# Optimization experiments

Hardware: AMD Instinct MI355X
Metric: run time of the kernel (lower is better)

The kernel has to match this reference:

```python
import jax, jax.numpy as jnp
import numpy as np

T = 200000


def _sine_layer(tvec, A, w, phi, phic, wc):
    # tvec: (t,), A/w/phi: (n,1), phic/wc: (1,)
    phi_static = jax.nn.relu(phic)  # (1,)
    w_static = jax.nn.relu(wc)
    ph = jax.nn.relu(phi) + phi_static  # (n,1)
    ww = jax.nn.relu(w) + w_static
    sine = A * jnp.sin(ww * tvec[None, :] + ph)  # (n,t)
    return sine, phi_static, w_static


def _selector_layer(tvec, wave_input, w, phi, phic, wc, phi_prev, w_prev):
    # wave_input: (n,t), w/phi: (m,n), phic/wc/phi_prev/w_prev: (1,)
    # NOTE: phi_prev/w_prev passed but phi_prev flag is False in the network,
    # so they are NOT added (matches torch: `if self.phi_prev and ...`).
    phi_static = jax.nn.relu(phic)
    w_static = jax.nn.relu(wc)
    ph = (jax.nn.relu(phi) + phi_static)[:, :, None]  # (m,n,1)
    ww = (jax.nn.relu(w) + w_static)[:, :, None]
    sine = 0.5 * jnp.sin(ww * tvec[None, None, :] + ph) + 0.5  # (m,n,t)
    out = jnp.einsum('mnt,nt->mt', sine, wave_input)  # (m,t)
    return out, phi_static, w_static


def setup_inputs() -> dict:
    key = jax.random.key(0)
    ks = jax.random.split(key, 18)
    r = lambda k, s: jax.random.normal(k, s, dtype=jnp.float32)
    return {
        'initial_wave_input': r(ks[0], (20, T)),
        'A0': r(ks[1], (20, 1)), 'w0': r(ks[2], (20, 1)), 'phi0': r(ks[3], (20, 1)),
        'wc0': r(ks[4], (1,)), 'phic0': r(ks[5], (1,)),
        'w1': r(ks[6], (25, 20)), 'phi1': r(ks[7], (25, 20)),
        'wc1': r(ks[8], (1,)), 'phic1': r(ks[9], (1,)),
        'w2': r(ks[10], (30, 25)), 'phi2': r(ks[11], (30, 25)),
        'wc2': r(ks[12], (1,)), 'phic2': r(ks[13], (1,)),
        'w3': r(ks[14], (1, 30)), 'phi3': r(ks[15], (1, 30)),
        'wc3': r(ks[16], (1,)), 'phic3': r(ks[17], (1,)),
    }


def reference(initial_wave_input, A0, w0, phi0, wc0, phic0,
              w1, phi1, wc1, phic1, w2, phi2, wc2, phic2,
              w3, phi3, wc3, phic3):
    tvec = jnp.linspace(1.0, 1000.0, T, dtype=jnp.float32)
    # initial_wave_input is an argument of the torch module but is never used.
    s, phi, w = _sine_layer(tvec, A0, w0, phi0, phic0, wc0)
    s, phi, w = _selector_layer(tvec, s, w1, phi1, phic1, wc1, phi, w)
    s, phi, w = _selector_layer(tvec, s, w2, phi2, phic2, wc2, phi, w)
    s, phi, w = _selector_layer(tvec, s, w3, phi3, phic3, wc3, phi, w)
    return s  # (1, t)
```

## Files before the change

### kernel.cpp

```cpp
#include <hip/hip_runtime.h>
#include <hip/hip_bf16.h>

#define T_TOTAL 200000
#define T_PAD   200192
#define STEPF   (999.0f / 199999.0f)

typedef float v4f __attribute__((ext_vector_type(4)));

__device__ float g_P[5200];
__device__ float g_s1[25 * T_PAD];

__device__ __forceinline__ float sinp(float rev) {
    float g = __builtin_amdgcn_fractf(rev);
    float h = g - 0.5f;
    float u = h * h;
    float p = fmaf(45.621248f, u, -82.391040f);
    p = fmaf(p, u, 64.671616f);
    p = fmaf(p, u, -19.730960f);
    p = fmaf(p, u, 0.9999618f);
    return p;
}

__global__ void prep_kernel(
    const float* __restrict__ A0,
    const float* __restrict__ w0, const float* __restrict__ phi0,
    const float* __restrict__ wc0, const float* __restrict__ phic0,
    const float* __restrict__ w1, const float* __restrict__ phi1,
    const float* __restrict__ wc1, const float* __restrict__ phic1,
    const float* __restrict__ w2, const float* __restrict__ phi2,
    const float* __restrict__ wc2, const float* __restrict__ phic2,
    const float* __restrict__ w3, const float* __restrict__ phi3,
    const float* __restrict__ wc3, const float* __restrict__ phic3)
{
    const int tid = blockIdx.x * blockDim.x + threadIdx.x;
    const int stride = blockDim.x * gridDim.x;

    const double I2PI = 0.15915494309189535;
    const double D1   = 999.0 / 199999.0;

    const double ws0 = fmax((double)wc0[0], 0.0), ps0 = fmax((double)phic0[0], 0.0);
    const double ws1 = fmax((double)wc1[0], 0.0), ps1 = fmax((double)phic1[0], 0.0);
    const double ws2 = fmax((double)wc2[0], 0.0), ps2 = fmax((double)phic2[0], 0.0);
    const double ws3 = fmax((double)wc3[0], 0.0), ps3 = fmax((double)phic3[0], 0.0);

    for (int n = tid; n < 20; n += stride) {
        double wr = fmax((double)w0[n], 0.0) + ws0;
        g_P[4 * n]     = (float)(wr * I2PI);
        g_P[4 * n + 1] = (float)((fmax((double)phi0[n], 0.0) + ps0) * I2PI + 0.25);
        g_P[4 * n + 2] = (float)(2.0 * cos(wr * D1));
        g_P[4 * n + 3] = A0[n];
    }
    for (int k = tid; k < 25 * 20; k += stride) {
        double wr = fmax((double)w1[k], 0.0) + ws1;
        g_P[80 + 4 * k]     = (float)(wr * I2PI);
        g_P[80 + 4 * k + 1] = (float)((fmax((double)phi1[k], 0.0) + ps1) * I2PI + 0.25);
        g_P[80 + 4 * k + 2] = (float)(2.0 * cos(wr * D1));
        g_P[80 + 4 * k + 3] = 0.0f;
    }
    for (int k = tid; k < 30 * 25; k += stride) {
        double wr = fmax((double)w2[k], 0.0) + ws2;
        g_P[2080 + 4 * k]     = (float)(wr * I2PI);
        g_P[2080 + 4 * k + 1] = (float)((fmax((double)phi2[k], 0.0) + ps2) * I2PI + 0.25);
        g_P[2080 + 4 * k + 2] = (float)(2.0 * cos(wr * D1));
        g_P[2080 + 4 * k + 3] = 0.0f;
    }
    for (int m = tid; m < 30; m += stride) {
        double wr = fmax((double)w3[m], 0.0) + ws3;
        g_P[5080 + 4 * m]     = (float)(wr * I2PI);
        g_P[5080 + 4 * m + 1] = (float)((fmax((double)phi3[m], 0.0) + ps3) * I2PI + 0.25);
        g_P[5080 + 4 * m + 2] = (float)(2.0 * cos(wr * D1));
        g_P[5080 + 4 * m + 3] = 0.0f;
    }
}

__launch_bounds__(256)
__global__ void k_l01()
{
    __shared__ float pp[2000];
    __shared__ float s0s[20 * 256];

    const int tid = threadIdx.x;
    for (int i = tid; i < 2000; i += 256) pp[i] = g_P[80 + i];

    const int l = tid & 63;
    const int w = __builtin_amdgcn_readfirstlane(tid >> 6);
    const int tb = blockIdx.x * 256;
    const int tl = 4 * l;
    const float tv0 = fmaf((float)(tb + tl), STEPF, 1.0f);
    const float tv1 = tv0 + STEPF;

#pragma unroll
    for (int i = 0; i < 5; ++i) {
        const int n = 5 * w + i;
        const v4f q = *(const v4f*)&g_P[4 * n];
        float x0 = q[3] * sinp(fmaf(q[0], tv0, q[1]));
        float x1 = q[3] * sinp(fmaf(q[0], tv1, q[1]));
        float x2 = fmaf(q[2], x1, -x0);
        float x3 = fmaf(q[2], x2, -x1);
        *(v4f*)&s0s[n * 256 + tl] = (v4f){x0, x1, x2, x3};
    }
    __syncthreads();

    float sum0[4] = {0.f, 0.f, 0.f, 0.f};
#pragma unroll
    for (int n = 0; n < 20; ++n) {
        const v4f s = *(const v4f*)&s0s[n * 256 + tl];
        sum0[0] += s[0]; sum0[1] += s[1]; sum0[2] += s[2]; sum0[3] += s[3];
    }

    const int mS = w ? (1 + 6 * w) : 0;
    const int mC = w ? 6 : 7;
    for (int i = 0; i < mC; ++i) {
        const int m = mS + i;
        const float* __restrict__ pb = &pp[80 * m];
        float a0 = 0.f, a1 = 0.f, a2 = 0.f, a3 = 0.f;
#pragma unroll
        for (int n = 0; n < 20; ++n) {
            const v4f q = *(const v4f*)&pb[4 * n];
            const v4f s = *(const v4f*)&s0s[n * 256 + tl];
            float x0 = sinp(fmaf(q[0], tv0, q[1]));
            float x1 = sinp(fmaf(q[0], tv1, q[1]));
            float x2 = fmaf(q[2], x1, -x0);
            float x3 = fmaf(q[2], x2, -x1);
            a0 = fmaf(x0, s[0], a0);
            a1 = fmaf(x1, s[1], a1);
            a2 = fmaf(x2, s[2], a2);
            a3 = fmaf(x3, s[3], a3);
        }
        const v4f o = {fmaf(0.5f, a0, 0.5f * sum0[0]),
                       fmaf(0.5f, a1, 0.5f * sum0[1]),
                       fmaf(0.5f, a2, 0.5f * sum0[2]),
                       fmaf(0.5f, a3, 0.5f * sum0[3])};
        *(v4f*)&g_s1[m * T_PAD + tb + tl] = o;
    }
}

__launch_bounds__(256)
__global__ void k_l23(float* __restrict__ out)
{
    __shared__ float pp[3120];
    __shared__ float s1s[25 * 256];

    const int tid = threadIdx.x;
    const int tb = blockIdx.x * 256;
    for (int i = tid; i < 3120; i += 256) pp[i] = g_P[2080 + i];
    for (int i = tid; i < 25 * 256; i += 256)
        s1s[i] = g_s1[(i >> 8) * T_PAD + tb + (i & 255)];
    __syncthreads();

    const int l = tid & 63;
    const int w = __builtin_amdgcn_readfirstlane(tid >> 6);
    const int tl = 4 * l;
    const float tv0 = fmaf((float)(tb + tl), STEPF, 1.0f);
    const float tv1 = tv0 + STEPF;

    float sum1[4] = {0.f, 0.f, 0.f, 0.f};
#pragma unroll
    for (int n = 0; n < 25; ++n) {
        const v4f s = *(const v4f*)&s1s[n * 256 + tl];
        sum1[0] += s[0]; sum1[1] += s[1]; sum1[2] += s[2]; sum1[3] += s[3];
    }

    const int mS = (w < 2) ? 8 * w : (16 + 7 * (w - 2));
    const int mC = (w < 2) ? 8 : 7;
    float pw0 = 0.f, pw1 = 0.f, pw2 = 0.f, pw3 = 0.f;
    for (int i = 0; i < mC; ++i) {
        const int m = mS + i;
        const float* __restrict__ pb = &pp[100 * m];
        float a0 = 0.f, a1 = 0.f, a2 = 0.f, a3 = 0.f;
#pragma unroll
        for (int n = 0; n < 25; ++n) {
            const v4f q = *(const v4f*)&pb[4 * n];
            const v4f s = *(const v4f*)&s1s[n * 256 + tl];
            float x0 = sinp(fmaf(q[0], tv0, q[1]));
            float x1 = sinp(fmaf(q[0], tv1, q[1]));
            float x2 = fmaf(q[2], x1, -x0);
            float x3 = fmaf(q[2], x2, -x1);
            a0 = fmaf(x0, s[0], a0);
            a1 = fmaf(x1, s[1], a1);
            a2 = fmaf(x2, s[2], a2);
            a3 = fmaf(x3, s[3], a3);
        }
        const v4f q3 = *(const v4f*)&pp[3000 + 4 * m];
        float y0 = sinp(fmaf(q3[0], tv0, q3[1]));
        float y1 = sinp(fmaf(q3[0], tv1, q3[1]));
        float y2 = fmaf(q3[2], y1, -y0);
        float y3 = fmaf(q3[2], y2, -y1);
        pw0 = fmaf(fmaf(0.5f, y0, 0.5f), fmaf(0.5f, a0, 0.5f * sum1[0]), pw0);
        pw1 = fmaf(fmaf(0.5f, y1, 0.5f), fmaf(0.5f, a1, 0.5f * sum1[1]), pw1);
        pw2 = fmaf(fmaf(0.5f, y2, 0.5f), fmaf(0.5f, a2, 0.5f * sum1[2]), pw2);
        pw3 = fmaf(fmaf(0.5f, y3, 0.5f), fmaf(0.5f, a3, 0.5f * sum1[3]), pw3);
    }
    __syncthreads();
    float* const shp = pp;
    *(v4f*)&shp[w * 256 + tl] = (v4f){pw0, pw1, pw2, pw3};
    __syncthreads();

    const int tlr = 64 * w + l;
    const float r = (shp[0 * 256 + tlr] + shp[1 * 256 + tlr])
                  + (shp[2 * 256 + tlr] + shp[3 * 256 + tlr]);
    const int tt = tb + tlr;
    if (tt < T_TOTAL) out[tt] = r;
}

extern "C" void kernel_launch(void* const* d_in, const int* in_sizes, int n_in,
                              void* d_out, int out_size, void* d_ws, size_t ws_size,
                              hipStream_t stream) {
    (void)in_sizes; (void)n_in; (void)d_ws; (void)ws_size; (void)out_size;
    const float* A0    = (const float*)d_in[1];
    const float* w0    = (const float*)d_in[2];
    const float* phi0  = (const float*)d_in[3];
    const float* wc0   = (const float*)d_in[4];
    const float* phic0 = (const float*)d_in[5];
    const float* w1    = (const float*)d_in[6];
    const float* phi1  = (const float*)d_in[7];
    const float* wc1   = (const float*)d_in[8];
    const float* phic1 = (const float*)d_in[9];
    const float* w2    = (const float*)d_in[10];
    const float* phi2  = (const float*)d_in[11];
    const float* wc2   = (const float*)d_in[12];
    const float* phic2 = (const float*)d_in[13];
    const float* w3    = (const float*)d_in[14];
    const float* phi3  = (const float*)d_in[15];
    const float* wc3   = (const float*)d_in[16];
    const float* phic3 = (const float*)d_in[17];

    float* out = (float*)d_out;

    hipLaunchKernelGGL(prep_kernel, dim3(6), dim3(256), 0, stream,
                       A0, w0, phi0, wc0, phic0,
                       w1, phi1, wc1, phic1,
                       w2, phi2, wc2, phic2,
                       w3, phi3, wc3, phic3);

    const int grid = (T_TOTAL + 255) / 256;
    hipLaunchKernelGGL(k_l01, dim3(grid), dim3(256), 0, stream);
    hipLaunchKernelGGL(k_l23, dim3(grid), dim3(256), 0, stream, out);
}
```

Measured before the change: 64.68 us.

## Split layer-2/3 kernel across two blocks per tile and combine partials

Each 256-element time tile of the layer-2/3 kernel is now handled by two blocks, each covering 15 of the 30 layer-2 outputs, with per-half partial sums written to a global buffer and added by a new combine kernel. The s1 tile is read directly from global memory instead of being staged in LDS, which shrinks shared memory use and should allow more resident blocks. This doubles the grid to fill more CUs, at the cost of an extra kernel launch, an extra global round trip for the partial sums, and redundant global loads of s1.

```diff
diff --git a/kernel.cpp b/kernel.cpp
--- a/kernel.cpp
+++ b/kernel.cpp
@@ -9,6 +9,7 @@
 
 __device__ float g_P[5200];
 __device__ float g_s1[25 * T_PAD];
+__device__ float g_part[2 * T_PAD];
 
 __device__ __forceinline__ float sinp(float rev) {
     float g = __builtin_amdgcn_fractf(rev);
@@ -136,17 +137,18 @@
 }
 
 __launch_bounds__(256)
-__global__ void k_l23(float* __restrict__ out)
-{
-    __shared__ float pp[3120];
-    __shared__ float s1s[25 * 256];
+__global__ void k_l23()
+{
+    __shared__ float pp[1560];
+    __shared__ float shp[4 * 256];
 
     const int tid = threadIdx.x;
-    const int tb = blockIdx.x * 256;
-    for (int i = tid; i < 3120; i += 256) pp[i] = g_P[2080 + i];
-    for (int i = tid; i < 25 * 256; i += 256)
-        s1s[i] = g_s1[(i >> 8) * T_PAD + tb + (i & 255)];
-    __syncthreads();
+    const int half = blockIdx.x & 1;
+    const int tb = (blockIdx.x >> 1) * 256;
+
+    for (int i = tid; i < 1560; i += 256)
+        pp[i] = (i < 1500) ? g_P[2080 + 1500 * half + i]
+                           : g_P[5080 + 60 * half + (i - 1500)];
 
     const int l = tid & 63;
     const int w = __builtin_amdgcn_readfirstlane(tid >> 6);
@@ -157,21 +159,22 @@
     float sum1[4] = {0.f, 0.f, 0.f, 0.f};
 #pragma unroll
     for (int n = 0; n < 25; ++n) {
-        const v4f s = *(const v4f*)&s1s[n * 256 + tl];
+        const v4f s = *(const v4f*)&g_s1[n * T_PAD + tb + tl];
         sum1[0] += s[0]; sum1[1] += s[1]; sum1[2] += s[2]; sum1[3] += s[3];
     }
-
-    const int mS = (w < 2) ? 8 * w : (16 + 7 * (w - 2));
-    const int mC = (w < 2) ? 8 : 7;
+    __syncthreads();
+
+    const int mS = 4 * w;
+    const int mC = (w == 3) ? 3 : 4;
     float pw0 = 0.f, pw1 = 0.f, pw2 = 0.f, pw3 = 0.f;
     for (int i = 0; i < mC; ++i) {
-        const int m = mS + i;
-        const float* __restrict__ pb = &pp[100 * m];
+        const int lm = mS + i;
+        const float* __restrict__ pb = &pp[100 * lm];
         float a0 = 0.f, a1 = 0.f, a2 = 0.f, a3 = 0.f;
 #pragma unroll
         for (int n = 0; n < 25; ++n) {
             const v4f q = *(const v4f*)&pb[4 * n];
-            const v4f s = *(const v4f*)&s1s[n * 256 + tl];
+            const v4f s = *(const v4f*)&g_s1[n * T_PAD + tb + tl];
             float x0 = sinp(fmaf(q[0], tv0, q[1]));
             float x1 = sinp(fmaf(q[0], tv1, q[1]));
             float x2 = fmaf(q[2], x1, -x0);
@@ -181,7 +184,7 @@
             a2 = fmaf(x2, s[2], a2);
             a3 = fmaf(x3, s[3], a3);
         }
-        const v4f q3 = *(const v4f*)&pp[3000 + 4 * m];
+        const v4f q3 = *(const v4f*)&pp[1500 + 4 * lm];
         float y0 = sinp(fmaf(q3[0], tv0, q3[1]));
         float y1 = sinp(fmaf(q3[0], tv1, q3[1]));
         float y2 = fmaf(q3[2], y1, -y0);
@@ -191,16 +194,19 @@
         pw2 = fmaf(fmaf(0.5f, y2, 0.5f), fmaf(0.5f, a2, 0.5f * sum1[2]), pw2);
         pw3 = fmaf(fmaf(0.5f, y3, 0.5f), fmaf(0.5f, a3, 0.5f * sum1[3]), pw3);
     }
-    __syncthreads();
-    float* const shp = pp;
     *(v4f*)&shp[w * 256 + tl] = (v4f){pw0, pw1, pw2, pw3};
     __syncthreads();
 
     const int tlr = 64 * w + l;
-    const float r = (shp[0 * 256 + tlr] + shp[1 * 256 + tlr])
-                  + (shp[2 * 256 + tlr] + shp[3 * 256 + tlr]);
-    const int tt = tb + tlr;
-    if (tt < T_TOTAL) out[tt] = r;
+    const float r = (shp[tlr] + shp[256 + tlr]) + (shp[512 + tlr] + shp[768 + tlr]);
+    g_part[half * T_PAD + tb + tlr] = r;
+}
+
+__launch_bounds__(256)
+__global__ void k_comb(float* __restrict__ out)
+{
+    const int t = blockIdx.x * 256 + threadIdx.x;
+    if (t < T_TOTAL) out[t] = g_part[t] + g_part[T_PAD + t];
 }
 
 extern "C" void kernel_launch(void* const* d_in, const int* in_sizes, int n_in,
@@ -235,5 +241,6 @@
 
     const int grid = (T_TOTAL + 255) / 256;
     hipLaunchKernelGGL(k_l01, dim3(grid), dim3(256), 0, stream);
-    hipLaunchKernelGGL(k_l23, dim3(grid), dim3(256), 0, stream, out);
-}
+    hipLaunchKernelGGL(k_l23, dim3(2 * grid), dim3(256), 0, stream);
+    hipLaunchKernelGGL(k_comb, dim3(grid), dim3(256), 0, stream, out);
+}
```

New measurement: 70.07 us. +8.3%, slower.

## Fuse layer-1 and layer-2/3 kernels into one, keeping intermediate in LDS

Applied to the files above, without the earlier changes.

Merges the two per-time-tile kernels into a single kernel that writes the 25-row layer-1 output to shared memory instead of a global scratch buffer, then reloads layer-2/3 parameters into reused LDS space. This removes a global write and read of the 25×T intermediate and one kernel launch. Shared memory per block grows to about 54 KB, which may reduce the number of resident blocks per CU.

```diff
diff --git a/kernel.cpp b/kernel.cpp
--- a/kernel.cpp
+++ b/kernel.cpp
@@ -2,13 +2,11 @@
 #include <hip/hip_bf16.h>
 
 #define T_TOTAL 200000
-#define T_PAD   200192
 #define STEPF   (999.0f / 199999.0f)
 
 typedef float v4f __attribute__((ext_vector_type(4)));
 
 __device__ float g_P[5200];
-__device__ float g_s1[25 * T_PAD];
 
 __device__ __forceinline__ float sinp(float rev) {
     float g = __builtin_amdgcn_fractf(rev);
@@ -74,14 +72,16 @@
 }
 
 __launch_bounds__(256)
-__global__ void k_l01()
+__global__ void wave_fused(float* __restrict__ out)
 {
-    __shared__ float pp[2000];
-    __shared__ float s0s[20 * 256];
+    __shared__ float S[13520];
+    float* const pp1 = S;
+    float* const s0s = S + 2000;
+    float* const s1s = S + 7120;
+    float* const pp2 = S;
+    float* const shp = S + 3200;
 
     const int tid = threadIdx.x;
-    for (int i = tid; i < 2000; i += 256) pp[i] = g_P[80 + i];
-
     const int l = tid & 63;
     const int w = __builtin_amdgcn_readfirstlane(tid >> 6);
     const int tb = blockIdx.x * 256;
@@ -89,6 +89,7 @@
     const float tv0 = fmaf((float)(tb + tl), STEPF, 1.0f);
     const float tv1 = tv0 + STEPF;
 
+    for (int i = tid; i < 2000; i += 256) pp1[i] = g_P[80 + i];
 #pragma unroll
     for (int i = 0; i < 5; ++i) {
         const int n = 5 * w + i;
@@ -107,52 +108,37 @@
         const v4f s = *(const v4f*)&s0s[n * 256 + tl];
         sum0[0] += s[0]; sum0[1] += s[1]; sum0[2] += s[2]; sum0[3] += s[3];
     }
-
-    const int mS = w ? (1 + 6 * w) : 0;
-    const int mC = w ? 6 : 7;
-    for (int i = 0; i < mC; ++i) {
-        const int m = mS + i;
-        const float* __restrict__ pb = &pp[80 * m];
-        float a0 = 0.f, a1 = 0.f, a2 = 0.f, a3 = 0.f;
-#pragma unroll
-        for (int n = 0; n < 20; ++n) {
-            const v4f q = *(const v4f*)&pb[4 * n];
-            const v4f s = *(const v4f*)&s0s[n * 256 + tl];
-            float x0 = sinp(fmaf(q[0], tv0, q[1]));
-            float x1 = sinp(fmaf(q[0], tv1, q[1]));
-            float x2 = fmaf(q[2], x1, -x0);
-            float x3 = fmaf(q[2], x2, -x1);
-            a0 = fmaf(x0, s[0], a0);
-            a1 = fmaf(x1, s[1], a1);
-            a2 = fmaf(x2, s[2], a2);
-            a3 = fmaf(x3, s[3], a3);
+    {
+        const int mS = w ? (1 + 6 * w) : 0;
+        const int mC = w ? 6 : 7;
+        for (int i = 0; i < mC; ++i) {
+            const int m = mS + i;
+            const float* __restrict__ pb = &pp1[80 * m];
+            float a0 = 0.f, a1 = 0.f, a2 = 0.f, a3 = 0.f;
+#pragma unroll
+            for (int n = 0; n < 20; ++n) {
+                const v4f q = *(const v4f*)&pb[4 * n];
+                const v4f s = *(const v4f*)&s0s[n * 256 + tl];
+                float x0 = sinp(fmaf(q[0], tv0, q[1]));
+                float x1 = sinp(fmaf(q[0], tv1, q[1]));
+                float x2 = fmaf(q[2], x1, -x0);
+                float x3 = fmaf(q[2], x2, -x1);
+                a0 = fmaf(x0, s[0], a0);
+                a1 = fmaf(x1, s[1], a1);
+                a2 = fmaf(x2, s[2], a2);
+                a3 = fmaf(x3, s[3], a3);
+            }
+            *(v4f*)&s1s[m * 256 + tl] = (v4f){
+                fmaf(0.5f, a0, 0.5f * sum0[0]),
+                fmaf(0.5f, a1, 0.5f * sum0[1]),
+                fmaf(0.5f, a2, 0.5f * sum0[2]),
+                fmaf(0.5f, a3, 0.5f * sum0[3])};
         }
-        const v4f o = {fmaf(0.5f, a0, 0.5f * sum0[0]),
-                       fmaf(0.5f, a1, 0.5f * sum0[1]),
-                       fmaf(0.5f, a2, 0.5f * sum0[2]),
-                       fmaf(0.5f, a3, 0.5f * sum0[3])};
-        *(v4f*)&g_s1[m * T_PAD + tb + tl] = o;
-    }
-}
-
-__launch_bounds__(256)
-__global__ void k_l23(float* __restrict__ out)
-{
-    __shared__ float pp[3120];
-    __shared__ float s1s[25 * 256];
-
-    const int tid = threadIdx.x;
-    const int tb = blockIdx.x * 256;
-    for (int i = tid; i < 3120; i += 256) pp[i] = g_P[2080 + i];
-    for (int i = tid; i < 25 * 256; i += 256)
-        s1s[i] = g_s1[(i >> 8) * T_PAD + tb + (i & 255)];
-    __syncthreads();
-
-    const int l = tid & 63;
-    const int w = __builtin_amdgcn_readfirstlane(tid >> 6);
-    const int tl = 4 * l;
-    const float tv0 = fmaf((float)(tb + tl), STEPF, 1.0f);
-    const float tv1 = tv0 + STEPF;
+    }
+    __syncthreads();
+
+    for (int i = tid; i < 3120; i += 256) pp2[i] = g_P[2080 + i];
+    __syncthreads();
 
     float sum1[4] = {0.f, 0.f, 0.f, 0.f};
 #pragma unroll
@@ -160,45 +146,44 @@
         const v4f s = *(const v4f*)&s1s[n * 256 + tl];
         sum1[0] += s[0]; sum1[1] += s[1]; sum1[2] += s[2]; sum1[3] += s[3];
     }
-
-    const int mS = (w < 2) ? 8 * w : (16 + 7 * (w - 2));
-    const int mC = (w < 2) ? 8 : 7;
     float pw0 = 0.f, pw1 = 0.f, pw2 = 0.f, pw3 = 0.f;
-    for (int i = 0; i < mC; ++i) {
-        const int m = mS + i;
-        const float* __restrict__ pb = &pp[100 * m];
-        float a0 = 0.f, a1 = 0.f, a2 = 0.f, a3 = 0.f;
-#pragma unroll
-        for (int n = 0; n < 25; ++n) {
-            const v4f q = *(const v4f*)&pb[4 * n];
-            const v4f s = *(const v4f*)&s1s[n * 256 + tl];
-            float x0 = sinp(fmaf(q[0], tv0, q[1]));
-            float x1 = sinp(fmaf(q[0], tv1, q[1]));
-            float x2 = fmaf(q[2], x1, -x0);
-            float x3 = fmaf(q[2], x2, -x1);
-            a0 = fmaf(x0, s[0], a0);
-            a1 = fmaf(x1, s[1], a1);
-            a2 = fmaf(x2, s[2], a2);
-            a3 = fmaf(x3, s[3], a3);
+    {
+        const int mS = (w < 2) ? 8 * w : (16 + 7 * (w - 2));
+        const int mC = (w < 2) ? 8 : 7;
+        for (int i = 0; i < mC; ++i) {
+            const int m = mS + i;
+            const float* __restrict__ pb = &pp2[100 * m];
+            float a0 = 0.f, a1 = 0.f, a2 = 0.f, a3 = 0.f;
+#pragma unroll
+            for (int n = 0; n < 25; ++n) {
+                const v4f q = *(const v4f*)&pb[4 * n];
+                const v4f s = *(const v4f*)&s1s[n * 256 + tl];
+                float x0 = sinp(fmaf(q[0], tv0, q[1]));
+                float x1 = sinp(fmaf(q[0], tv1, q[1]));
+                float x2 = fmaf(q[2], x1, -x0);
+                float x3 = fmaf(q[2], x2, -x1);
+                a0 = fmaf(x0, s[0], a0);
+                a1 = fmaf(x1, s[1], a1);
+                a2 = fmaf(x2, s[2], a2);
+                a3 = fmaf(x3, s[3], a3);
+            }
+            const v4f q3 = *(const v4f*)&pp2[3000 + 4 * m];
+            float y0 = sinp(fmaf(q3[0], tv0, q3[1]));
+            float y1 = sinp(fmaf(q3[0], tv1, q3[1]));
+            float y2 = fmaf(q3[2], y1, -y0);
+            float y3 = fmaf(q3[2], y2, -y1);
+            pw0 = fmaf(fmaf(0.5f, y0, 0.5f), fmaf(0.5f, a0, 0.5f * sum1[0]), pw0);
+            pw1 = fmaf(fmaf(0.5f, y1, 0.5f), fmaf(0.5f, a1, 0.5f * sum1[1]), pw1);
+            pw2 = fmaf(fmaf(0.5f, y2, 0.5f), fmaf(0.5f, a2, 0.5f * sum1[2]), pw2);
+            pw3 = fmaf(fmaf(0.5f, y3, 0.5f), fmaf(0.5f, a3, 0.5f * sum1[3]), pw3);
         }
-        const v4f q3 = *(const v4f*)&pp[3000 + 4 * m];
-        float y0 = sinp(fmaf(q3[0], tv0, q3[1]));
-        float y1 = sinp(fmaf(q3[0], tv1, q3[1]));
-        float y2 = fmaf(q3[2], y1, -y0);
-        float y3 = fmaf(q3[2], y2, -y1);
-        pw0 = fmaf(fmaf(0.5f, y0, 0.5f), fmaf(0.5f, a0, 0.5f * sum1[0]), pw0);
-        pw1 = fmaf(fmaf(0.5f, y1, 0.5f), fmaf(0.5f, a1, 0.5f * sum1[1]), pw1);
-        pw2 = fmaf(fmaf(0.5f, y2, 0.5f), fmaf(0.5f, a2, 0.5f * sum1[2]), pw2);
-        pw3 = fmaf(fmaf(0.5f, y3, 0.5f), fmaf(0.5f, a3, 0.5f * sum1[3]), pw3);
-    }
-    __syncthreads();
-    float* const shp = pp;
+    }
+    __syncthreads();
     *(v4f*)&shp[w * 256 + tl] = (v4f){pw0, pw1, pw2, pw3};
     __syncthreads();
 
     const int tlr = 64 * w + l;
-    const float r = (shp[0 * 256 + tlr] + shp[1 * 256 + tlr])
-                  + (shp[2 * 256 + tlr] + shp[3 * 256 + tlr]);
+    const float r = (shp[tlr] + shp[256 + tlr]) + (shp[512 + tlr] + shp[768 + tlr]);
     const int tt = tb + tlr;
     if (tt < T_TOTAL) out[tt] = r;
 }
@@ -234,6 +219,5 @@
                        w3, phi3, wc3, phic3);
 
     const int grid = (T_TOTAL + 255) / 256;
-    hipLaunchKernelGGL(k_l01, dim3(grid), dim3(256), 0, stream);
-    hipLaunchKernelGGL(k_l23, dim3(grid), dim3(256), 0, stream, out);
-}
+    hipLaunchKernelGGL(wave_fused, dim3(grid), dim3(256), 0, stream, out);
+}
```

Result: faster. 57.60 us (-11.0%).
